# Optimization experiments

Measured on AMD Instinct MI355X. Metric: run time of the kernel, lower is better.

## Reference

```python
import jax, jax.numpy as jnp
import numpy as np

NE = 200000   # num_entities
NR = 16       # num_relations
D  = 128      # embed_dim
B  = 4096     # batch
S  = 64       # neighbors per node
L  = 2        # num_layers
H  = 4        # attention heads (hardcoded in module)


def _ln(x, g, b, eps=1e-5):
    m = jnp.mean(x, -1, keepdims=True)
    v = jnp.mean((x - m) ** 2, -1, keepdims=True)
    return (x - m) * jax.lax.rsqrt(v + eps) * g + b


def setup_inputs() -> dict:
    key = jax.random.key(0)
    ks = jax.random.split(key, 12)
    s = 0.05
    return {
        'drug_entity_indices': jax.random.randint(ks[0], (B,), 0, NE),
        'adj_entity': jax.random.randint(ks[1], (B, S), 0, NE),
        'adj_relation': jax.random.randint(ks[2], (B, S), 0, NR),
        'edge_weights': jax.random.uniform(ks[3], (B, S), dtype=jnp.float32),
        'entity_emb': jax.random.normal(ks[4], (NE, D), jnp.float32) * s,
        'W_rgcn': jax.random.normal(ks[5], (L, NR, D, D), jnp.float32) * s,
        'res_w': jax.random.normal(ks[6], (L, D, D), jnp.float32) * s,
        'res_b': jnp.zeros((L, D), jnp.float32),
        'proj_w': jax.random.normal(ks[7], (L, D, D), jnp.float32) * s,
        'proj_b': jnp.zeros((L, D), jnp.float32),
        'ln_g': jnp.ones((L, D), jnp.float32),
        'ln_b': jnp.zeros((L, D), jnp.float32),
        'in_proj_w': jax.random.normal(ks[8], (3 * D, D), jnp.float32) * s,
        'in_proj_b': jnp.zeros((3 * D,), jnp.float32),
        'out_proj_w': jax.random.normal(ks[9], (D, D), jnp.float32) * s,
        'out_proj_b': jnp.zeros((D,), jnp.float32),
        'fln_g': jnp.ones((D,), jnp.float32),
        'fln_b': jnp.zeros((D,), jnp.float32),
    }


def reference(drug_entity_indices, adj_entity, adj_relation, edge_weights,
              entity_emb, W_rgcn, res_w, res_b, proj_w, proj_b, ln_g, ln_b,
              in_proj_w, in_proj_b, out_proj_w, out_proj_b, fln_g, fln_b):
    node = entity_emb[drug_entity_indices]           # [B,D] combined_emb
    nbr = entity_emb[adj_entity]                     # [B,S,D]
    # Route each edge to its relation: sum_s nbr*ew*[rel==r] then one GEMM per relation
    # (mathematically identical to the per-relation masked matmul loop in torch).
    onehot = jax.nn.one_hot(adj_relation, NR, dtype=node.dtype)      # [B,S,R]
    pre = jnp.einsum('bsd,bsr->brd', nbr * edge_weights[..., None], onehot)
    outs = []
    for l in range(L):
        msgs = jnp.einsum('brd,rde->be', pre, W_rgcn[l])             # [B,D]
        h = jax.nn.relu(node + msgs + node @ res_w[l].T + res_b[l])  # RGCNAggregator
        node = _ln(h @ proj_w[l].T + proj_b[l] + node, ln_g[l], ln_b[l])
        outs.append(node)
    x = jnp.stack(outs, 0)                           # [L,B,D] seq-first
    qkv = x @ in_proj_w.T + in_proj_b
    q, k, v = jnp.split(qkv, 3, axis=-1)
    hd = D // H
    def heads(t):
        return t.reshape(L, B, H, hd).transpose(1, 2, 0, 3)          # [B,H,L,hd]
    q, k, v = heads(q), heads(k), heads(v)
    att = jax.nn.softmax(jnp.einsum('bhld,bhmd->bhlm', q, k) / np.sqrt(hd).astype(np.float32), axis=-1)
    o = jnp.einsum('bhlm,bhmd->bhld', att, v).transpose(2, 0, 1, 3).reshape(L, B, D)
    o = o @ out_proj_w.T + out_proj_b
    return _ln(o.mean(0), fln_g, fln_b)              # [B,D]
```

## Files before the change

kernel.cpp:

```cpp
#include <hip/hip_runtime.h>
#include <math.h>

#define NRREL 16
#define DDIM 128
#define BBATCH 4096
#define SNBR 64

typedef __attribute__((ext_vector_type(8))) short short8;
typedef __attribute__((ext_vector_type(4))) float floatx4;

__device__ __forceinline__ unsigned short f2bf(float f) {
    unsigned u = __builtin_bit_cast(unsigned, f);
    u += 0x7fffu + ((u >> 16) & 1u);
    return (unsigned short)(u >> 16);
}
__device__ __forceinline__ float bf2f(unsigned short u) {
    return __builtin_bit_cast(float, ((unsigned)u) << 16);
}

extern "C" __global__ __launch_bounds__(256)
void k_prep(const float* __restrict__ W_rgcn,
            const float* __restrict__ res_w, const float* __restrict__ proj_w,
            const float* __restrict__ in_w, const float* __restrict__ out_w,
            unsigned short* __restrict__ Wcat, unsigned short* __restrict__ resw,
            unsigned short* __restrict__ projw, unsigned short* __restrict__ inw,
            unsigned short* __restrict__ outw)
{
    __shared__ float tileT[64 * 65];
    const int bid = blockIdx.x, t = threadIdx.x;

    if (bid < 128) {
        const int l = bid >> 6, rem = bid & 63;
        const int k0 = (rem >> 1) * 64, e0 = (rem & 1) * 64;
        #pragma unroll
        for (int i = 0; i < 4; ++i) {
            int flat = t + 256 * i;
            int k = flat >> 4, c = flat & 15;
            float4 v = *(const float4*)(W_rgcn + ((size_t)(l * 2048 + k0 + k)) * 128 + e0 + 4 * c);
            tileT[(4 * c + 0) * 65 + k] = v.x;
            tileT[(4 * c + 1) * 65 + k] = v.y;
            tileT[(4 * c + 2) * 65 + k] = v.z;
            tileT[(4 * c + 3) * 65 + k] = v.w;
        }
        __syncthreads();
        const int e = t >> 2, m = t & 3;
        #pragma unroll
        for (int half = 0; half < 2; ++half) {
            int kk = 16 * m + 8 * half;
            short8 o;
            #pragma unroll
            for (int j = 0; j < 8; ++j) o[j] = (short)f2bf(tileT[e * 65 + kk + j]);
            *(short8*)(Wcat + ((size_t)(l * 128 + e0 + e)) * 2048 + k0 + kk) = o;
        }
    } else {
        int j4 = ((bid - 128) * 256 + t) * 4;
        const float* src; unsigned short* dst; int off;
        if (j4 < 32768)       { src = res_w;  dst = resw;  off = j4; }
        else if (j4 < 65536)  { src = proj_w; dst = projw; off = j4 - 32768; }
        else if (j4 < 114688) { src = in_w;   dst = inw;   off = j4 - 65536; }
        else                  { src = out_w;  dst = outw;  off = j4 - 114688; }
        float4 v = *(const float4*)(src + off);
        ushort4 o = { f2bf(v.x), f2bf(v.y), f2bf(v.z), f2bf(v.w) };
        *(ushort4*)(dst + off) = o;
    }
}

extern "C" __global__ __launch_bounds__(512)
void k_fused(const int* __restrict__ drug, const int* __restrict__ adj_e,
             const int* __restrict__ adj_r, const float* __restrict__ ew,
             const float* __restrict__ emb,
             const unsigned short* __restrict__ Wcat,
             const unsigned short* __restrict__ resw, const unsigned short* __restrict__ projw,
             const float* __restrict__ res_b, const float* __restrict__ proj_b,
             const float* __restrict__ ln_g, const float* __restrict__ ln_b,
             const unsigned short* __restrict__ inw, const float* __restrict__ in_b,
             const unsigned short* __restrict__ outw, const float* __restrict__ out_b,
             const float* __restrict__ fg, const float* __restrict__ fb,
             float* __restrict__ outp)
{
    __shared__ union {
        struct { unsigned short preA[16 * 2056]; } a;
        struct {
            unsigned short h_b16[16 * 136];
            unsigned short xs_l[32 * 136];
            unsigned short qkvl[32 * 392];
        } t;
    } sm;
    __shared__ float node_ln[16 * 132];
    __shared__ unsigned short node_b16[16 * 136];
    __shared__ union {
        struct {
            int   cnt[16][16];
            int   strt[16][16];
            int   sperm[16][64];
            float wperm[16][64];
        } g;
        float msum[16 * 260];
    } sg;
    __shared__ float psum[8][16], psq[8][16];

    const int t = threadIdx.x, w = t >> 6, lane = t & 63, l15 = lane & 15, q = lane >> 4;
    const int r0 = blockIdx.x * 16;

    const int erow = t >> 6, es = t & 63;
    int   ent0 = adj_e[(r0 + erow) * SNBR + es];
    float ewt0 = ew[(r0 + erow) * SNBR + es];
    int   rel0 = adj_r[(r0 + erow) * SNBR + es];
    int   ent1 = adj_e[(r0 + erow + 8) * SNBR + es];
    float ewt1 = ew[(r0 + erow + 8) * SNBR + es];
    int   rel1 = adj_r[(r0 + erow + 8) * SNBR + es];
    if (t < 256) sg.g.cnt[t >> 4][t & 15] = 0;
    {
        int rr = t >> 5, c = t & 31;
        int di = drug[r0 + rr];
        float4 v = *(const float4*)(emb + (size_t)di * DDIM + 4 * c);
        *(float4*)(node_ln + rr * 132 + 4 * c) = v;
        ushort4 o = { f2bf(v.x), f2bf(v.y), f2bf(v.z), f2bf(v.w) };
        *(ushort4*)(node_b16 + rr * 136 + 4 * c) = o;
    }
    __syncthreads();

    atomicAdd(&sg.g.cnt[erow][rel0], 1);
    atomicAdd(&sg.g.cnt[erow + 8][rel1], 1);
    __syncthreads();

    if (t < 16) {
        int a = 0;
        #pragma unroll
        for (int r = 0; r < NRREL; ++r) { sg.g.strt[t][r] = a; a += sg.g.cnt[t][r]; }
    }
    __syncthreads();

    {
        int pos0 = atomicAdd(&sg.g.strt[erow][rel0], 1);
        sg.g.sperm[erow][pos0] = ent0;
        sg.g.wperm[erow][pos0] = ewt0;
        int pos1 = atomicAdd(&sg.g.strt[erow + 8][rel1], 1);
        sg.g.sperm[erow + 8][pos1] = ent1;
        sg.g.wperm[erow + 8][pos1] = ewt1;
    }
    __syncthreads();

    {
        const int h = t >> 8, tt = t & 255;
        const int rl = tt >> 4, g8 = tt & 15;
        #pragma unroll 1
        for (int p = 0; p < 8; ++p) {
            int row = 2 * p + h;
            int n = sg.g.cnt[row][rl];
            int end = sg.g.strt[row][rl];
            int beg = end - n;
            float acc[8] = {0.f, 0.f, 0.f, 0.f, 0.f, 0.f, 0.f, 0.f};
            #pragma unroll 1
            for (int jb = beg; jb < end; jb += 8) {
                const float* pp[8]; float wq[8];
                #pragma unroll
                for (int u = 0; u < 8; ++u) {
                    int live = (jb + u < end);
                    int j = live ? jb + u : beg;
                    wq[u] = live ? sg.g.wperm[row][j] : 0.f;
                    pp[u] = emb + (size_t)sg.g.sperm[row][j] * DDIM + 8 * g8;
                }
                float4 v0[8], v1[8];
                #pragma unroll
                for (int u = 0; u < 8; ++u) {
                    v0[u] = *(const float4*)pp[u];
                    v1[u] = *(const float4*)(pp[u] + 4);
                }
                #pragma unroll
                for (int u = 0; u < 8; ++u) {
                    acc[0] = fmaf(v0[u].x, wq[u], acc[0]); acc[1] = fmaf(v0[u].y, wq[u], acc[1]);
                    acc[2] = fmaf(v0[u].z, wq[u], acc[2]); acc[3] = fmaf(v0[u].w, wq[u], acc[3]);
                    acc[4] = fmaf(v1[u].x, wq[u], acc[4]); acc[5] = fmaf(v1[u].y, wq[u], acc[5]);
                    acc[6] = fmaf(v1[u].z, wq[u], acc[6]); acc[7] = fmaf(v1[u].w, wq[u], acc[7]);
                }
            }
            short8 o;
            #pragma unroll
            for (int jj = 0; jj < 8; ++jj) o[jj] = (short)f2bf(acc[jj]);
            *(short8*)(sm.a.preA + row * 2056 + rl * DDIM + 8 * g8) = o;
        }
    }
    __syncthreads();

    {
        floatx4 macc[2] = {};
        const unsigned short* ap = sm.a.preA + l15 * 2056 + 8 * q;
        const unsigned short* bp = Wcat + (size_t)(32 * w + l15) * 2048 + 8 * q;
        #pragma unroll 8
        for (int k = 0; k < 2048; k += 32) {
            short8 A = *(const short8*)(ap + k);
            #pragma unroll
            for (int ni = 0; ni < 2; ++ni) {
                short8 B = *(const short8*)(bp + (size_t)(ni * 16) * 2048 + k);
                macc[ni] = __builtin_amdgcn_mfma_f32_16x16x32_bf16(A, B, macc[ni], 0, 0, 0);
            }
        }
        #pragma unroll
        for (int ni = 0; ni < 2; ++ni) {
            int gc = 32 * w + ni * 16 + l15;
            #pragma unroll
            for (int r = 0; r < 4; ++r)
                sg.msum[(4 * q + r) * 260 + gc] = macc[ni][r];
        }
    }
    __syncthreads();

    for (int l = 0; l < 2; ++l) {
        {
            const unsigned short* Bw = resw + (size_t)l * DDIM * DDIM;
            floatx4 acc = {};
            const unsigned short* ap = node_b16 + l15 * 136 + 8 * q;
            #pragma unroll
            for (int kk = 0; kk < DDIM; kk += 32) {
                short8 A = *(const short8*)(ap + kk);
                short8 B = *(const short8*)(Bw + (size_t)(16 * w + l15) * DDIM + kk + 8 * q);
                acc = __builtin_amdgcn_mfma_f32_16x16x32_bf16(A, B, acc, 0, 0, 0);
            }
            int gc = 16 * w + l15;
            float rb = res_b[l * DDIM + gc];
            #pragma unroll
            for (int r = 0; r < 4; ++r) {
                int lr = 4 * q + r;
                float v = acc[r] + rb + node_ln[lr * 132 + gc] + sg.msum[lr * 260 + l * DDIM + gc];
                sm.t.h_b16[lr * 136 + gc] = f2bf(v > 0.f ? v : 0.f);
            }
        }
        __syncthreads();
        {
            const unsigned short* Bw = projw + (size_t)l * DDIM * DDIM;
            floatx4 acc = {};
            const unsigned short* ap = sm.t.h_b16 + l15 * 136 + 8 * q;
            #pragma unroll
            for (int kk = 0; kk < DDIM; kk += 32) {
                short8 A = *(const short8*)(ap + kk);
                short8 B = *(const short8*)(Bw + (size_t)(16 * w + l15) * DDIM + kk + 8 * q);
                acc = __builtin_amdgcn_mfma_f32_16x16x32_bf16(A, B, acc, 0, 0, 0);
            }
            int gc = 16 * w + l15;
            float vv[4];
            float s4[4] = {0, 0, 0, 0}, sq4[4] = {0, 0, 0, 0};
            float pb = proj_b[l * DDIM + gc];
            #pragma unroll
            for (int r = 0; r < 4; ++r) {
                int lr = 4 * q + r;
                float v = acc[r] + pb + node_ln[lr * 132 + gc];
                vv[r] = v; s4[r] += v; sq4[r] += v * v;
            }
            #pragma unroll
            for (int r = 0; r < 4; ++r)
                #pragma unroll
                for (int off2 = 8; off2 >= 1; off2 >>= 1) {
                    s4[r] += __shfl_xor(s4[r], off2, 64);
                    sq4[r] += __shfl_xor(sq4[r], off2, 64);
                }
            if (l15 == 0) {
                #pragma unroll
                for (int r = 0; r < 4; ++r) {
                    psum[w][4 * q + r] = s4[r];
                    psq[w][4 * q + r] = sq4[r];
                }
            }
            __syncthreads();
            float g2 = ln_g[l * DDIM + gc], bb = ln_b[l * DDIM + gc];
            #pragma unroll
            for (int r = 0; r < 4; ++r) {
                int lr = 4 * q + r;
                float ssum = 0.f, ssq = 0.f;
                #pragma unroll
                for (int ww = 0; ww < 8; ++ww) { ssum += psum[ww][lr]; ssq += psq[ww][lr]; }
                float mean = ssum * (1.f / DDIM);
                float var = ssq * (1.f / DDIM) - mean * mean;
                float val = (vv[r] - mean) * rsqrtf(var + 1e-5f) * g2 + bb;
                node_ln[lr * 132 + gc] = val;
                unsigned short ub = f2bf(val);
                node_b16[lr * 136 + gc] = ub;
                sm.t.xs_l[(2 * lr + l) * 136 + gc] = ub;
            }
            __syncthreads();
        }
    }

    {
        floatx4 acc[6] = {};
        const unsigned short* ap = sm.t.xs_l + (16 * (w & 1) + l15) * 136 + 8 * q;
        #pragma unroll
        for (int kk = 0; kk < DDIM; kk += 32) {
            short8 A = *(const short8*)(ap + kk);
            #pragma unroll
            for (int ni = 0; ni < 6; ++ni) {
                short8 B = *(const short8*)(inw + (size_t)(96 * (w >> 1) + ni * 16 + l15) * DDIM + kk + 8 * q);
                acc[ni] = __builtin_amdgcn_mfma_f32_16x16x32_bf16(A, B, acc[ni], 0, 0, 0);
            }
        }
        #pragma unroll
        for (int ni = 0; ni < 6; ++ni) {
            int gc = 96 * (w >> 1) + ni * 16 + l15;
            float ib = in_b[gc];
            #pragma unroll
            for (int r = 0; r < 4; ++r)
                sm.t.qkvl[(16 * (w & 1) + 4 * q + r) * 392 + gc] = f2bf(acc[ni][r] + ib);
        }
    }
    __syncthreads();

    if (t < 128) {
        int g4 = t >> 3, j = t & 7;
        const unsigned short* row0 = sm.t.qkvl + (2 * g4) * 392;
        const unsigned short* row1 = row0 + 392;
        float p00 = 0.f, p01 = 0.f, p10 = 0.f, p11 = 0.f;
        #pragma unroll
        for (int dd = 0; dd < 16; ++dd) {
            int d = 16 * j + dd;
            float q0 = bf2f(row0[d]), k0 = bf2f(row0[128 + d]);
            float q1 = bf2f(row1[d]), k1 = bf2f(row1[128 + d]);
            p00 = fmaf(q0, k0, p00); p01 = fmaf(q0, k1, p01);
            p10 = fmaf(q1, k0, p10); p11 = fmaf(q1, k1, p11);
        }
        p00 += __shfl_xor(p00, 1, 64); p01 += __shfl_xor(p01, 1, 64);
        p10 += __shfl_xor(p10, 1, 64); p11 += __shfl_xor(p11, 1, 64);
        const float sc = 0.17677669529663687f;
        p00 *= sc; p01 *= sc; p10 *= sc; p11 *= sc;
        float m0 = fmaxf(p00, p01), e00 = expf(p00 - m0), e01 = expf(p01 - m0);
        float i0 = 1.f / (e00 + e01);
        float m1 = fmaxf(p10, p11), e10 = expf(p10 - m1), e11 = expf(p11 - m1);
        float i1 = 1.f / (e10 + e11);
        #pragma unroll
        for (int dd = 0; dd < 16; ++dd) {
            int d = 16 * j + dd;
            float v0 = bf2f(row0[256 + d]), v1 = bf2f(row1[256 + d]);
            sm.t.xs_l[(2 * g4) * 136 + d]     = f2bf((e00 * v0 + e01 * v1) * i0);
            sm.t.xs_l[(2 * g4 + 1) * 136 + d] = f2bf((e10 * v0 + e11 * v1) * i1);
        }
    }
    __syncthreads();

    {
        floatx4 acc[2] = {};
        const unsigned short* ap = sm.t.xs_l + (16 * (w & 1) + l15) * 136 + 8 * q;
        #pragma unroll
        for (int kk = 0; kk < DDIM; kk += 32) {
            short8 A = *(const short8*)(ap + kk);
            #pragma unroll
            for (int ni = 0; ni < 2; ++ni) {
                short8 B = *(const short8*)(outw + (size_t)(32 * (w >> 1) + ni * 16 + l15) * DDIM + kk + 8 * q);
                acc[ni] = __builtin_amdgcn_mfma_f32_16x16x32_bf16(A, B, acc[ni], 0, 0, 0);
            }
        }
        float av[2][2];
        float s2[2] = {0, 0}, sq2[2] = {0, 0};
        #pragma unroll
        for (int ni = 0; ni < 2; ++ni) {
            int gc = 32 * (w >> 1) + ni * 16 + l15;
            float ob = out_b[gc];
            #pragma unroll
            for (int rr = 0; rr < 2; ++rr) {
                float v = 0.5f * (acc[ni][2 * rr] + acc[ni][2 * rr + 1]) + ob;
                av[ni][rr] = v; s2[rr] += v; sq2[rr] += v * v;
            }
        }
        #pragma unroll
        for (int rr = 0; rr < 2; ++rr)
            #pragma unroll
            for (int off2 = 8; off2 >= 1; off2 >>= 1) {
                s2[rr] += __shfl_xor(s2[rr], off2, 64);
                sq2[rr] += __shfl_xor(sq2[rr], off2, 64);
            }
        if (l15 == 0) {
            #pragma unroll
            for (int rr = 0; rr < 2; ++rr) {
                psum[w][2 * q + rr] = s2[rr];
                psq[w][2 * q + rr] = sq2[rr];
            }
        }
        __syncthreads();
        #pragma unroll
        for (int ni = 0; ni < 2; ++ni) {
            int gc = 32 * (w >> 1) + ni * 16 + l15;
            float g2 = fg[gc], bb = fb[gc];
            #pragma unroll
            for (int rr = 0; rr < 2; ++rr) {
                int idx = 2 * q + rr;
                int bl = 8 * (w & 1) + idx;
                float ssum = psum[w & 1][idx] + psum[(w & 1) + 2][idx]
                           + psum[(w & 1) + 4][idx] + psum[(w & 1) + 6][idx];
                float ssq  = psq[w & 1][idx] + psq[(w & 1) + 2][idx]
                           + psq[(w & 1) + 4][idx] + psq[(w & 1) + 6][idx];
                float mean = ssum * (1.f / DDIM);
                float var = ssq * (1.f / DDIM) - mean * mean;
                outp[(size_t)(r0 + bl) * DDIM + gc] = (av[ni][rr] - mean) * rsqrtf(var + 1e-5f) * g2 + bb;
            }
        }
    }
}

extern "C" void kernel_launch(void* const* d_in, const int* in_sizes, int n_in,
                              void* d_out, int out_size, void* d_ws, size_t ws_size,
                              hipStream_t stream) {
    const int*   drug_idx = (const int*)d_in[0];
    const int*   adj_ent  = (const int*)d_in[1];
    const int*   adj_rel  = (const int*)d_in[2];
    const float* ew       = (const float*)d_in[3];
    const float* emb      = (const float*)d_in[4];
    const float* W_rgcn   = (const float*)d_in[5];
    const float* res_w    = (const float*)d_in[6];
    const float* res_b    = (const float*)d_in[7];
    const float* proj_w   = (const float*)d_in[8];
    const float* proj_b   = (const float*)d_in[9];
    const float* ln_g     = (const float*)d_in[10];
    const float* ln_b     = (const float*)d_in[11];
    const float* in_w     = (const float*)d_in[12];
    const float* in_b     = (const float*)d_in[13];
    const float* out_w    = (const float*)d_in[14];
    const float* out_b    = (const float*)d_in[15];
    const float* fg       = (const float*)d_in[16];
    const float* fb       = (const float*)d_in[17];
    float* outp = (float*)d_out;

    char* ws = (char*)d_ws;
    size_t off = 0;
    auto alloc = [&](size_t bytes) { size_t o = off; off = (off + bytes + 255) & ~(size_t)255; return o; };
    unsigned short* Wcat    = (unsigned short*)(ws + alloc((size_t)256 * 2048 * 2));
    unsigned short* resw    = (unsigned short*)(ws + alloc((size_t)2 * 128 * 128 * 2));
    unsigned short* projw   = (unsigned short*)(ws + alloc((size_t)2 * 128 * 128 * 2));
    unsigned short* inw     = (unsigned short*)(ws + alloc((size_t)384 * 128 * 2));
    unsigned short* outw    = (unsigned short*)(ws + alloc((size_t)128 * 128 * 2));

    hipLaunchKernelGGL(k_prep, dim3(256), dim3(256), 0, stream,
                       W_rgcn, res_w, proj_w, in_w, out_w,
                       Wcat, resw, projw, inw, outw);
    hipLaunchKernelGGL(k_fused, dim3(256), dim3(512), 0, stream,
                       drug_idx, adj_ent, adj_rel, ew, emb,
                       Wcat, resw, projw, res_b, proj_b, ln_g, ln_b,
                       inw, in_b, outw, out_b, fg, fb, outp);
}
```

Baseline: 231.2 us.

## Halve rows per block to launch 512 blocks and fill more CUs

Each block now handles 8 batch rows instead of 16, so the fused kernel launches 512 blocks instead of 256, which gives the 256 CUs more work and more latency hiding during the random embedding gather. The per-row work mapping is reworked to fit: gather loops are remapped, 16-row MFMA tiles read duplicated rows and throw away the upper half, and the QKV and output-projection thread splits change. In exchange, half the MFMA work in the dense stages is wasted, and the 16x2048 relation-weight matrix is streamed from cache by twice as many blocks.

Result: slower. 261.9 us (+13.3%).

```diff
diff --git a/kernel.cpp b/kernel.cpp
--- a/kernel.cpp
+++ b/kernel.cpp
@@ -5,6 +5,7 @@
 #define DDIM 128
 #define BBATCH 4096
 #define SNBR 64
+#define ROWS 8
 
 typedef __attribute__((ext_vector_type(8))) short short8;
 typedef __attribute__((ext_vector_type(4))) float floatx4;
@@ -79,38 +80,35 @@
              float* __restrict__ outp)
 {
     __shared__ union {
-        struct { unsigned short preA[16 * 2056]; } a;
+        struct { unsigned short preA[ROWS * 2056]; } a;
         struct {
-            unsigned short h_b16[16 * 136];
-            unsigned short xs_l[32 * 136];
-            unsigned short qkvl[32 * 392];
+            unsigned short h_b16[ROWS * 136];
+            unsigned short xs_l[2 * ROWS * 136];
+            unsigned short qkvl[2 * ROWS * 392];
         } t;
     } sm;
-    __shared__ float node_ln[16 * 132];
-    __shared__ unsigned short node_b16[16 * 136];
+    __shared__ float node_ln[ROWS * 132];
+    __shared__ unsigned short node_b16[ROWS * 136];
     __shared__ union {
         struct {
-            int   cnt[16][16];
-            int   strt[16][16];
-            int   sperm[16][64];
-            float wperm[16][64];
+            int   cnt[ROWS][16];
+            int   strt[ROWS][16];
+            int   sperm[ROWS][64];
+            float wperm[ROWS][64];
         } g;
-        float msum[16 * 260];
+        float msum[ROWS * 260];
     } sg;
-    __shared__ float psum[8][16], psq[8][16];
+    __shared__ float psum[8][8], psq[8][8];
 
     const int t = threadIdx.x, w = t >> 6, lane = t & 63, l15 = lane & 15, q = lane >> 4;
-    const int r0 = blockIdx.x * 16;
+    const int r0 = blockIdx.x * ROWS;
 
     const int erow = t >> 6, es = t & 63;
     int   ent0 = adj_e[(r0 + erow) * SNBR + es];
     float ewt0 = ew[(r0 + erow) * SNBR + es];
     int   rel0 = adj_r[(r0 + erow) * SNBR + es];
-    int   ent1 = adj_e[(r0 + erow + 8) * SNBR + es];
-    float ewt1 = ew[(r0 + erow + 8) * SNBR + es];
-    int   rel1 = adj_r[(r0 + erow + 8) * SNBR + es];
-    if (t < 256) sg.g.cnt[t >> 4][t & 15] = 0;
-    {
+    if (t < 128) sg.g.cnt[t >> 4][t & 15] = 0;
+    if (t < 256) {
         int rr = t >> 5, c = t & 31;
         int di = drug[r0 + rr];
         float4 v = *(const float4*)(emb + (size_t)di * DDIM + 4 * c);
@@ -121,10 +119,9 @@
     __syncthreads();
 
     atomicAdd(&sg.g.cnt[erow][rel0], 1);
-    atomicAdd(&sg.g.cnt[erow + 8][rel1], 1);
-    __syncthreads();
-
-    if (t < 16) {
+    __syncthreads();
+
+    if (t < ROWS) {
         int a = 0;
         #pragma unroll
         for (int r = 0; r < NRREL; ++r) { sg.g.strt[t][r] = a; a += sg.g.cnt[t][r]; }
@@ -135,18 +132,14 @@
         int pos0 = atomicAdd(&sg.g.strt[erow][rel0], 1);
         sg.g.sperm[erow][pos0] = ent0;
         sg.g.wperm[erow][pos0] = ewt0;
-        int pos1 = atomicAdd(&sg.g.strt[erow + 8][rel1], 1);
-        sg.g.sperm[erow + 8][pos1] = ent1;
-        sg.g.wperm[erow + 8][pos1] = ewt1;
     }
     __syncthreads();
 
     {
-        const int h = t >> 8, tt = t & 255;
-        const int rl = tt >> 4, g8 = tt & 15;
         #pragma unroll 1
-        for (int p = 0; p < 8; ++p) {
-            int row = 2 * p + h;
+        for (int i = 0; i < 4; ++i) {
+            int u = t + 512 * i;
+            int row = u >> 8, rl = (u >> 4) & 15, g8 = u & 15;
             int n = sg.g.cnt[row][rl];
             int end = sg.g.strt[row][rl];
             int beg = end - n;
@@ -155,24 +148,24 @@
             for (int jb = beg; jb < end; jb += 8) {
                 const float* pp[8]; float wq[8];
                 #pragma unroll
-                for (int u = 0; u < 8; ++u) {
-                    int live = (jb + u < end);
-                    int j = live ? jb + u : beg;
-                    wq[u] = live ? sg.g.wperm[row][j] : 0.f;
-                    pp[u] = emb + (size_t)sg.g.sperm[row][j] * DDIM + 8 * g8;
+                for (int u2 = 0; u2 < 8; ++u2) {
+                    int live = (jb + u2 < end);
+                    int j = live ? jb + u2 : beg;
+                    wq[u2] = live ? sg.g.wperm[row][j] : 0.f;
+                    pp[u2] = emb + (size_t)sg.g.sperm[row][j] * DDIM + 8 * g8;
                 }
                 float4 v0[8], v1[8];
                 #pragma unroll
-                for (int u = 0; u < 8; ++u) {
-                    v0[u] = *(const float4*)pp[u];
-                    v1[u] = *(const float4*)(pp[u] + 4);
-                }
-                #pragma unroll
-                for (int u = 0; u < 8; ++u) {
-                    acc[0] = fmaf(v0[u].x, wq[u], acc[0]); acc[1] = fmaf(v0[u].y, wq[u], acc[1]);
-                    acc[2] = fmaf(v0[u].z, wq[u], acc[2]); acc[3] = fmaf(v0[u].w, wq[u], acc[3]);
-                    acc[4] = fmaf(v1[u].x, wq[u], acc[4]); acc[5] = fmaf(v1[u].y, wq[u], acc[5]);
-                    acc[6] = fmaf(v1[u].z, wq[u], acc[6]); acc[7] = fmaf(v1[u].w, wq[u], acc[7]);
+                for (int u2 = 0; u2 < 8; ++u2) {
+                    v0[u2] = *(const float4*)pp[u2];
+                    v1[u2] = *(const float4*)(pp[u2] + 4);
+                }
+                #pragma unroll
+                for (int u2 = 0; u2 < 8; ++u2) {
+                    acc[0] = fmaf(v0[u2].x, wq[u2], acc[0]); acc[1] = fmaf(v0[u2].y, wq[u2], acc[1]);
+                    acc[2] = fmaf(v0[u2].z, wq[u2], acc[2]); acc[3] = fmaf(v0[u2].w, wq[u2], acc[3]);
+                    acc[4] = fmaf(v1[u2].x, wq[u2], acc[4]); acc[5] = fmaf(v1[u2].y, wq[u2], acc[5]);
+                    acc[6] = fmaf(v1[u2].z, wq[u2], acc[6]); acc[7] = fmaf(v1[u2].w, wq[u2], acc[7]);
                 }
             }
             short8 o;
@@ -185,7 +178,7 @@
 
     {
         floatx4 macc[2] = {};
-        const unsigned short* ap = sm.a.preA + l15 * 2056 + 8 * q;
+        const unsigned short* ap = sm.a.preA + (l15 & 7) * 2056 + 8 * q;
         const unsigned short* bp = Wcat + (size_t)(32 * w + l15) * 2048 + 8 * q;
         #pragma unroll 8
         for (int k = 0; k < 2048; k += 32) {
@@ -196,12 +189,14 @@
                 macc[ni] = __builtin_amdgcn_mfma_f32_16x16x32_bf16(A, B, macc[ni], 0, 0, 0);
             }
         }
-        #pragma unroll
-        for (int ni = 0; ni < 2; ++ni) {
-            int gc = 32 * w + ni * 16 + l15;
-            #pragma unroll
-            for (int r = 0; r < 4; ++r)
-                sg.msum[(4 * q + r) * 260 + gc] = macc[ni][r];
+        if (q < 2) {
+            #pragma unroll
+            for (int ni = 0; ni < 2; ++ni) {
+                int gc = 32 * w + ni * 16 + l15;
+                #pragma unroll
+                for (int r = 0; r < 4; ++r)
+                    sg.msum[(4 * q + r) * 260 + gc] = macc[ni][r];
+            }
         }
     }
     __syncthreads();
@@ -210,7 +205,7 @@
         {
             const unsigned short* Bw = resw + (size_t)l * DDIM * DDIM;
             floatx4 acc = {};
-            const unsigned short* ap = node_b16 + l15 * 136 + 8 * q;
+            const unsigned short* ap = node_b16 + (l15 & 7) * 136 + 8 * q;
             #pragma unroll
             for (int kk = 0; kk < DDIM; kk += 32) {
                 short8 A = *(const short8*)(ap + kk);
@@ -219,18 +214,20 @@
             }
             int gc = 16 * w + l15;
             float rb = res_b[l * DDIM + gc];
-            #pragma unroll
-            for (int r = 0; r < 4; ++r) {
-                int lr = 4 * q + r;
-                float v = acc[r] + rb + node_ln[lr * 132 + gc] + sg.msum[lr * 260 + l * DDIM + gc];
-                sm.t.h_b16[lr * 136 + gc] = f2bf(v > 0.f ? v : 0.f);
+            if (q < 2) {
+                #pragma unroll
+                for (int r = 0; r < 4; ++r) {
+                    int lr = 4 * q + r;
+                    float v = acc[r] + rb + node_ln[lr * 132 + gc] + sg.msum[lr * 260 + l * DDIM + gc];
+                    sm.t.h_b16[lr * 136 + gc] = f2bf(v > 0.f ? v : 0.f);
+                }
             }
         }
         __syncthreads();
         {
             const unsigned short* Bw = projw + (size_t)l * DDIM * DDIM;
             floatx4 acc = {};
-            const unsigned short* ap = sm.t.h_b16 + l15 * 136 + 8 * q;
+            const unsigned short* ap = sm.t.h_b16 + (l15 & 7) * 136 + 8 * q;
             #pragma unroll
             for (int kk = 0; kk < DDIM; kk += 32) {
                 short8 A = *(const short8*)(ap + kk);
@@ -241,11 +238,12 @@
             float vv[4];
             float s4[4] = {0, 0, 0, 0}, sq4[4] = {0, 0, 0, 0};
             float pb = proj_b[l * DDIM + gc];
-            #pragma unroll
-            for (int r = 0; r < 4; ++r) {
-                int lr = 4 * q + r;
-                float v = acc[r] + pb + node_ln[lr * 132 + gc];
-                vv[r] = v; s4[r] += v; sq4[r] += v * v;
+            if (q < 2) {
+                #pragma unroll
+                for (int r = 0; r < 4; ++r) {
+                    float v = acc[r] + pb + node_ln[(4 * q + r) * 132 + gc];
+                    vv[r] = v; s4[r] = v; sq4[r] = v * v;
+                }
             }
             #pragma unroll
             for (int r = 0; r < 4; ++r)
@@ -254,7 +252,7 @@
                     s4[r] += __shfl_xor(s4[r], off2, 64);
                     sq4[r] += __shfl_xor(sq4[r], off2, 64);
                 }
-            if (l15 == 0) {
+            if (l15 == 0 && q < 2) {
                 #pragma unroll
                 for (int r = 0; r < 4; ++r) {
                     psum[w][4 * q + r] = s4[r];
@@ -263,48 +261,50 @@
             }
             __syncthreads();
             float g2 = ln_g[l * DDIM + gc], bb = ln_b[l * DDIM + gc];
-            #pragma unroll
-            for (int r = 0; r < 4; ++r) {
-                int lr = 4 * q + r;
-                float ssum = 0.f, ssq = 0.f;
-                #pragma unroll
-                for (int ww = 0; ww < 8; ++ww) { ssum += psum[ww][lr]; ssq += psq[ww][lr]; }
-                float mean = ssum * (1.f / DDIM);
-                float var = ssq * (1.f / DDIM) - mean * mean;
-                float val = (vv[r] - mean) * rsqrtf(var + 1e-5f) * g2 + bb;
-                node_ln[lr * 132 + gc] = val;
-                unsigned short ub = f2bf(val);
-                node_b16[lr * 136 + gc] = ub;
-                sm.t.xs_l[(2 * lr + l) * 136 + gc] = ub;
+            if (q < 2) {
+                #pragma unroll
+                for (int r = 0; r < 4; ++r) {
+                    int lr = 4 * q + r;
+                    float ssum = 0.f, ssq = 0.f;
+                    #pragma unroll
+                    for (int ww = 0; ww < 8; ++ww) { ssum += psum[ww][lr]; ssq += psq[ww][lr]; }
+                    float mean = ssum * (1.f / DDIM);
+                    float var = ssq * (1.f / DDIM) - mean * mean;
+                    float val = (vv[r] - mean) * rsqrtf(var + 1e-5f) * g2 + bb;
+                    node_ln[lr * 132 + gc] = val;
+                    unsigned short ub = f2bf(val);
+                    node_b16[lr * 136 + gc] = ub;
+                    sm.t.xs_l[(2 * lr + l) * 136 + gc] = ub;
+                }
             }
             __syncthreads();
         }
     }
 
     {
-        floatx4 acc[6] = {};
-        const unsigned short* ap = sm.t.xs_l + (16 * (w & 1) + l15) * 136 + 8 * q;
+        floatx4 acc[3] = {};
+        const unsigned short* ap = sm.t.xs_l + l15 * 136 + 8 * q;
         #pragma unroll
         for (int kk = 0; kk < DDIM; kk += 32) {
             short8 A = *(const short8*)(ap + kk);
             #pragma unroll
-            for (int ni = 0; ni < 6; ++ni) {
-                short8 B = *(const short8*)(inw + (size_t)(96 * (w >> 1) + ni * 16 + l15) * DDIM + kk + 8 * q);
+            for (int ni = 0; ni < 3; ++ni) {
+                short8 B = *(const short8*)(inw + (size_t)(48 * w + ni * 16 + l15) * DDIM + kk + 8 * q);
                 acc[ni] = __builtin_amdgcn_mfma_f32_16x16x32_bf16(A, B, acc[ni], 0, 0, 0);
             }
         }
         #pragma unroll
-        for (int ni = 0; ni < 6; ++ni) {
-            int gc = 96 * (w >> 1) + ni * 16 + l15;
+        for (int ni = 0; ni < 3; ++ni) {
+            int gc = 48 * w + ni * 16 + l15;
             float ib = in_b[gc];
             #pragma unroll
             for (int r = 0; r < 4; ++r)
-                sm.t.qkvl[(16 * (w & 1) + 4 * q + r) * 392 + gc] = f2bf(acc[ni][r] + ib);
-        }
-    }
-    __syncthreads();
-
-    if (t < 128) {
+                sm.t.qkvl[(4 * q + r) * 392 + gc] = f2bf(acc[ni][r] + ib);
+        }
+    }
+    __syncthreads();
+
+    if (t < 64) {
         int g4 = t >> 3, j = t & 7;
         const unsigned short* row0 = sm.t.qkvl + (2 * g4) * 392;
         const unsigned short* row1 = row0 + 392;
@@ -336,28 +336,22 @@
     __syncthreads();
 
     {
-        floatx4 acc[2] = {};
-        const unsigned short* ap = sm.t.xs_l + (16 * (w & 1) + l15) * 136 + 8 * q;
+        floatx4 acc = {};
+        const unsigned short* ap = sm.t.xs_l + l15 * 136 + 8 * q;
         #pragma unroll
         for (int kk = 0; kk < DDIM; kk += 32) {
             short8 A = *(const short8*)(ap + kk);
-            #pragma unroll
-            for (int ni = 0; ni < 2; ++ni) {
-                short8 B = *(const short8*)(outw + (size_t)(32 * (w >> 1) + ni * 16 + l15) * DDIM + kk + 8 * q);
-                acc[ni] = __builtin_amdgcn_mfma_f32_16x16x32_bf16(A, B, acc[ni], 0, 0, 0);
-            }
-        }
-        float av[2][2];
-        float s2[2] = {0, 0}, sq2[2] = {0, 0};
-        #pragma unroll
-        for (int ni = 0; ni < 2; ++ni) {
-            int gc = 32 * (w >> 1) + ni * 16 + l15;
-            float ob = out_b[gc];
-            #pragma unroll
-            for (int rr = 0; rr < 2; ++rr) {
-                float v = 0.5f * (acc[ni][2 * rr] + acc[ni][2 * rr + 1]) + ob;
-                av[ni][rr] = v; s2[rr] += v; sq2[rr] += v * v;
-            }
+            short8 B = *(const short8*)(outw + (size_t)(16 * w + l15) * DDIM + kk + 8 * q);
+            acc = __builtin_amdgcn_mfma_f32_16x16x32_bf16(A, B, acc, 0, 0, 0);
+        }
+        int gc = 16 * w + l15;
+        float ob = out_b[gc];
+        float av[2];
+        float s2[2], sq2[2];
+        #pragma unroll
+        for (int rr = 0; rr < 2; ++rr) {
+            float v = 0.5f * (acc[2 * rr] + acc[2 * rr + 1]) + ob;
+            av[rr] = v; s2[rr] = v; sq2[rr] = v * v;
         }
         #pragma unroll
         for (int rr = 0; rr < 2; ++rr)
@@ -374,22 +368,16 @@
             }
         }
         __syncthreads();
-        #pragma unroll
-        for (int ni = 0; ni < 2; ++ni) {
-            int gc = 32 * (w >> 1) + ni * 16 + l15;
-            float g2 = fg[gc], bb = fb[gc];
-            #pragma unroll
-            for (int rr = 0; rr < 2; ++rr) {
-                int idx = 2 * q + rr;
-                int bl = 8 * (w & 1) + idx;
-                float ssum = psum[w & 1][idx] + psum[(w & 1) + 2][idx]
-                           + psum[(w & 1) + 4][idx] + psum[(w & 1) + 6][idx];
-                float ssq  = psq[w & 1][idx] + psq[(w & 1) + 2][idx]
-                           + psq[(w & 1) + 4][idx] + psq[(w & 1) + 6][idx];
-                float mean = ssum * (1.f / DDIM);
-                float var = ssq * (1.f / DDIM) - mean * mean;
-                outp[(size_t)(r0 + bl) * DDIM + gc] = (av[ni][rr] - mean) * rsqrtf(var + 1e-5f) * g2 + bb;
-            }
+        float g2 = fg[gc], bb = fb[gc];
+        #pragma unroll
+        for (int rr = 0; rr < 2; ++rr) {
+            int idx = 2 * q + rr;
+            float ssum = 0.f, ssq = 0.f;
+            #pragma unroll
+            for (int ww = 0; ww < 8; ++ww) { ssum += psum[ww][idx]; ssq += psq[ww][idx]; }
+            float mean = ssum * (1.f / DDIM);
+            float var = ssq * (1.f / DDIM) - mean * mean;
+            outp[(size_t)(r0 + idx) * DDIM + gc] = (av[rr] - mean) * rsqrtf(var + 1e-5f) * g2 + bb;
         }
     }
 }
@@ -429,7 +417,7 @@
     hipLaunchKernelGGL(k_prep, dim3(256), dim3(256), 0, stream,
                        W_rgcn, res_w, proj_w, in_w, out_w,
                        Wcat, resw, projw, inw, outw);
-    hipLaunchKernelGGL(k_fused, dim3(256), dim3(512), 0, stream,
+    hipLaunchKernelGGL(k_fused, dim3(BBATCH / ROWS), dim3(512), 0, stream,
                        drug_idx, adj_ent, adj_rel, ew, emb,
                        Wcat, resw, projw, res_b, proj_b, ln_g, ln_b,
                        inw, in_b, outw, out_b, fg, fb, outp);
```
